# Optimization experiments

Hardware: AMD Instinct MI355X
Metric: run time of the kernel (lower is better)

The kernel has to match this reference:

```python
import jax, jax.numpy as jnp
import numpy as np

B = 1024        # number of dialogs
MX_LEN = 110    # max utterances per dialog (alpha width hardcoded to 110 in source)
G_DIM = 512     # node feature dim
WP, WF = 10, 10 # past / future window
ALPHA_W = 110
NEG = -1e9


def setup_inputs() -> dict:
    key = jax.random.key(0)
    k1, k2, k3 = jax.random.split(key, 3)
    node_features = jax.random.normal(k1, (B, MX_LEN, G_DIM), dtype=jnp.float32)
    var = 2.0 / (G_DIM + G_DIM)  # matches torch init: normal_(0, var)
    weight = jax.random.normal(k2, (G_DIM, G_DIM), dtype=jnp.float32) * var
    text_len = jax.random.randint(k3, (B,), 1, MX_LEN + 1)
    return {"node_features": node_features, "weight": weight, "text_len": text_len}


def reference(node_features, weight, text_len):
    Bsz, L, D = node_features.shape
    # att_matrix[b, l] = weight @ node_features[b, l]
    att = jnp.einsum('de,ble->bld', weight, node_features)            # [B, L, D]
    # score[b, j, l] = att[b, l] . node_features[b, j]
    scores = jnp.einsum('bld,bjd->bjl', att, node_features)           # [B, J, Lkey]
    j = jnp.arange(L)[:, None]   # query position
    l = jnp.arange(L)[None, :]   # key position
    lens = text_len[:, None, None]                                    # [B, 1, 1]
    # window: s = max(0, j-wp), e = min(j+wf, cur_len-1); valid only for j < cur_len
    mask = (l >= j - WP) & (l <= j + WF) & (l <= lens - 1) & (j <= lens - 1)
    probs = jax.nn.softmax(jnp.where(mask, scores, NEG), axis=-1)
    probs = jnp.where(mask, probs, 0.0)                               # [B, L, L]
    # alpha is [mx_len, 110] per batch, zero outside window; stack over batch
    alpha = jnp.zeros((Bsz, L, ALPHA_W), dtype=probs.dtype).at[:, :, :L].set(probs)
    return alpha
```

## Files before the change

### kernel.cpp

```cpp
#include <hip/hip_runtime.h>
#include <stdint.h>

#define L_SZ 110
#define D_SZ 512
#define OUT_W 110
#define A_STRIDE 520
#define C_STRIDE 136
#define A_ROWS 112
#define ATT_ROWS 112
#define G3_ST 40

typedef __attribute__((ext_vector_type(8))) __bf16 bf16x8;
typedef __attribute__((ext_vector_type(4))) __bf16 bf16x4;
typedef __attribute__((ext_vector_type(4))) float f32x4;

__global__ __launch_bounds__(256) void wconv_kernel(const float* __restrict__ W,
                                                    __bf16* __restrict__ wbf) {
    int idx = blockIdx.x * 256 + threadIdx.x;
    float4 w = ((const float4*)W)[idx];
    bf16x4 o;
    o[0] = (__bf16)w.x; o[1] = (__bf16)w.y; o[2] = (__bf16)w.z; o[3] = (__bf16)w.w;
    ((bf16x4*)wbf)[idx] = o;
}

__global__ __launch_bounds__(256, 3) void att_gemm3_kernel(
    const float* __restrict__ nf, const __bf16* __restrict__ wbf,
    const int* __restrict__ tlenp, __bf16* __restrict__ attws)
{
    __shared__ __bf16 A_lds[112 * G3_ST];
    __shared__ __bf16 B_lds[128 * G3_ST];

    const int b   = blockIdx.y;
    const int cg  = blockIdx.x;
    const int tid = threadIdx.x;
    const int lane = tid & 63;
    const int wave = tid >> 6;
    const int l15  = lane & 15;
    const int quad = lane >> 4;

    int len = tlenp[b];
    if (len > L_SZ) len = L_SZ;
    if (len < 1) len = 1;
    const int T = (len + 15) >> 4;
    const int rows_needed = T << 4;

    const float* nfb = nf + (size_t)b * (L_SZ * D_SZ);

    const int r0 = tid >> 2;
    const int c8 = (tid & 3) << 3;
    const int rows2[2] = { r0, r0 + 64 };
    int stat[2];
    #pragma unroll
    for (int s = 0; s < 2; ++s) {
        int r = rows2[s];
        stat[s] = (r >= rows_needed) ? 0 : ((r < L_SZ) ? 1 : 2);
    }

    f32x4 acc[7][2];
    const f32x4 fz = {0.f, 0.f, 0.f, 0.f};
    #pragma unroll
    for (int m = 0; m < 7; ++m) { acc[m][0] = fz; acc[m][1] = fz; }

    float4 abuf[2][2];
    bf16x8 bbuf[2];

    auto load_tiles = [&](int k0) {
        #pragma unroll
        for (int s = 0; s < 2; ++s) {
            if (stat[s] == 1) {
                const float* ap = nfb + (size_t)rows2[s] * D_SZ + k0 + c8;
                abuf[s][0] = *(const float4*)ap;
                abuf[s][1] = *(const float4*)(ap + 4);
            }
            bbuf[s] = *(const bf16x8*)&wbf[(size_t)(cg * 128 + rows2[s]) * D_SZ + k0 + c8];
        }
    };
    auto store_tiles = [&]() {
        #pragma unroll
        for (int s = 0; s < 2; ++s) {
            if (stat[s]) {
                bf16x8 o;
                if (stat[s] == 1) {
                    o[0]=(__bf16)abuf[s][0].x; o[1]=(__bf16)abuf[s][0].y;
                    o[2]=(__bf16)abuf[s][0].z; o[3]=(__bf16)abuf[s][0].w;
                    o[4]=(__bf16)abuf[s][1].x; o[5]=(__bf16)abuf[s][1].y;
                    o[6]=(__bf16)abuf[s][1].z; o[7]=(__bf16)abuf[s][1].w;
                } else {
                    o[0]=o[1]=o[2]=o[3]=o[4]=o[5]=o[6]=o[7]=(__bf16)0.0f;
                }
                *(bf16x8*)&A_lds[rows2[s] * G3_ST + c8] = o;
            }
            *(bf16x8*)&B_lds[rows2[s] * G3_ST + c8] = bbuf[s];
        }
    };

    load_tiles(0);
    for (int kt = 0; kt < 16; ++kt) {
        store_tiles();
        __syncthreads();
        if (kt < 15) load_tiles((kt + 1) << 5);
        bf16x8 bfr[2];
        #pragma unroll
        for (int ni = 0; ni < 2; ++ni)
            bfr[ni] = *(const bf16x8*)&B_lds[(wave * 32 + ni * 16 + l15) * G3_ST + quad * 8];
        #pragma unroll
        for (int m = 0; m < 7; ++m) {
            if (m < T) {
                bf16x8 af = *(const bf16x8*)&A_lds[(m * 16 + l15) * G3_ST + quad * 8];
                acc[m][0] = __builtin_amdgcn_mfma_f32_16x16x32_bf16(af, bfr[0], acc[m][0], 0, 0, 0);
                acc[m][1] = __builtin_amdgcn_mfma_f32_16x16x32_bf16(af, bfr[1], acc[m][1], 0, 0, 0);
            }
        }
        __syncthreads();
    }

    __bf16* tw = &A_lds[wave * 16 * G3_ST];
    const size_t obase = (size_t)b * (ATT_ROWS * D_SZ) + cg * 128 + wave * 32;
    const int erow = lane >> 2;
    const int ec8  = (lane & 3) << 3;
    #pragma unroll
    for (int m = 0; m < 7; ++m) {
        if (m < T) {
            #pragma unroll
            for (int ni = 0; ni < 2; ++ni)
                #pragma unroll
                for (int r = 0; r < 4; ++r)
                    tw[(quad * 4 + r) * G3_ST + ni * 16 + l15] = (__bf16)acc[m][ni][r];
            bf16x8 v = *(const bf16x8*)&tw[erow * G3_ST + ec8];
            *(bf16x8*)&attws[obase + (size_t)(m * 16 + erow) * D_SZ + ec8] = v;
        }
    }
}

__global__ __launch_bounds__(256) void band_kernel(
    const float* __restrict__ nf, const __bf16* __restrict__ attws,
    const int* __restrict__ tlenp, float* __restrict__ out)
{
    const int b = blockIdx.x;
    const int tid = threadIdx.x;
    const int lane = tid & 63;
    const int wave = tid >> 6;
    const int l15 = lane & 15;
    const int quad = lane >> 4;

    int len = tlenp[b];
    if (len > L_SZ) len = L_SZ;
    if (len < 1) len = 1;
    const int T = (len + 15) >> 4;

    const float* nfb = nf + (size_t)b * (L_SZ * D_SZ);
    float* outb = out + (size_t)b * (L_SZ * OUT_W);

    const f32x4 fz = {0.f, 0.f, 0.f, 0.f};
    f32x4 accS[2][3];
    #pragma unroll
    for (int i = 0; i < 2; ++i)
        #pragma unroll
        for (int t = 0; t < 3; ++t) accS[i][t] = fz;

    #pragma unroll
    for (int i = 0; i < 2; ++i) {
        const int tj = wave + (i << 2);
        if (tj < T) {
            int jr = (tj << 4) + l15;
            if (jr > L_SZ - 1) jr = L_SZ - 1;
            const float* ap0 = &nfb[(size_t)jr * D_SZ];
            for (int k0 = 0; k0 < D_SZ; k0 += 32) {
                float4 a0 = *(const float4*)(ap0 + k0 + (quad << 3));
                float4 a1 = *(const float4*)(ap0 + k0 + (quad << 3) + 4);
                bf16x8 af;
                af[0] = (__bf16)a0.x; af[1] = (__bf16)a0.y;
                af[2] = (__bf16)a0.z; af[3] = (__bf16)a0.w;
                af[4] = (__bf16)a1.x; af[5] = (__bf16)a1.y;
                af[6] = (__bf16)a1.z; af[7] = (__bf16)a1.w;
                #pragma unroll
                for (int t = 0; t < 3; ++t) {
                    int tl = tj - 1 + t;
                    if (tl >= 0 && tl < T) {
                        bf16x8 bfr = *(const bf16x8*)&attws[((size_t)b * ATT_ROWS + (tl << 4) + l15) * D_SZ + k0 + (quad << 3)];
                        accS[i][t] = __builtin_amdgcn_mfma_f32_16x16x32_bf16(
                            af, bfr, accS[i][t], 0, 0, 0);
                    }
                }
            }
        }
    }

    #pragma unroll
    for (int i = 0; i < 2; ++i) {
        int tj = wave + 4 * i;
        if (tj >= T) continue;
        #pragma unroll
        for (int r = 0; r < 4; ++r) {
            int j = tj * 16 + quad * 4 + r;
            float v[3]; bool mk[3];
            float vmax = -3.0e38f;
            #pragma unroll
            for (int t = 0; t < 3; ++t) {
                int tl = tj - 1 + t;
                int l = tl * 16 + l15;
                bool in = (tl >= 0) && (tl < T) && (j < len) && (l < len)
                          && (l >= j - 10) && (l <= j + 10);
                float val = in ? accS[i][t][r] : -3.0e38f;
                mk[t] = in; v[t] = val;
                vmax = fmaxf(vmax, val);
            }
            #pragma unroll
            for (int s = 1; s < 16; s <<= 1)
                vmax = fmaxf(vmax, __shfl_xor(vmax, s, 16));
            float e[3]; float esum = 0.f;
            #pragma unroll
            for (int t = 0; t < 3; ++t) {
                e[t] = mk[t] ? __expf(v[t] - vmax) : 0.f;
                esum += e[t];
            }
            #pragma unroll
            for (int s = 1; s < 16; s <<= 1)
                esum += __shfl_xor(esum, s, 16);
            float inv = (esum > 0.f) ? (1.0f / esum) : 0.f;
            if (j < OUT_W) {
                #pragma unroll
                for (int t = 0; t < 3; ++t) {
                    int tl = tj - 1 + t;
                    if (tl >= 0 && tl < T) {
                        int l = tl * 16 + l15;
                        if (l < OUT_W) outb[(size_t)j * OUT_W + l] = e[t] * inv;
                    }
                }
            }
        }
    }
}

__global__ __launch_bounds__(256, 1) void edgeatt_kernel(
    const float* __restrict__ nf, const float* __restrict__ Wf,
    const __bf16* __restrict__ wbf, const int* __restrict__ tlenp,
    float* __restrict__ out, int use_wb)
{
    __shared__ __bf16 A_lds[A_ROWS * A_STRIDE];
    __shared__ __bf16 C_lds[A_ROWS * C_STRIDE];

    const int b = blockIdx.x;
    const int tid = threadIdx.x;
    const int lane = tid & 63;
    const int wave = tid >> 6;
    const int l15 = lane & 15;
    const int quad = lane >> 4;

    int len = tlenp[b];
    if (len > L_SZ) len = L_SZ;
    if (len < 1) len = 1;
    const int T = (len + 15) >> 4;

    const float* nfb = nf + (size_t)b * (L_SZ * D_SZ);
    float* outb = out + (size_t)b * (L_SZ * OUT_W);

    {
        int total4 = len * (D_SZ / 4);
        for (int idx = tid; idx < total4; idx += 256) {
            int row = idx >> 7;
            int c4 = idx & 127;
            float4 v = ((const float4*)nfb)[row * 128 + c4];
            bf16x4 o;
            o[0]=(__bf16)v.x; o[1]=(__bf16)v.y; o[2]=(__bf16)v.z; o[3]=(__bf16)v.w;
            *(bf16x4*)&A_lds[row * A_STRIDE + c4 * 4] = o;
        }
        int zr = 16 * T - len;
        if (zr > 0) {
            int per = A_STRIDE / 4;
            int totalz = zr * per;
            for (int idx = tid; idx < totalz; idx += 256) {
                int row = len + idx / per;
                int c4 = idx % per;
                bf16x4 z; z[0]=z[1]=z[2]=z[3]=(__bf16)0.0f;
                *(bf16x4*)&A_lds[row * A_STRIDE + c4 * 4] = z;
            }
        }
    }
    __syncthreads();

    const int wm = wave >> 1, wn = wave & 1;
    const int h = (T + 1) >> 1;
    const int mt_lo = (wm == 0) ? 0 : h;
    const int nmt = ((wm == 0) ? h : T) - mt_lo;

    const f32x4 fzero = {0.f, 0.f, 0.f, 0.f};
    f32x4 accS[2][3];
    #pragma unroll
    for (int i = 0; i < 2; ++i)
        #pragma unroll
        for (int t = 0; t < 3; ++t) accS[i][t] = fzero;

    for (int c = 0; c < 4; ++c) {
        const int d0 = c * 128;
        f32x4 acc1[4][4];
        #pragma unroll
        for (int mi = 0; mi < 4; ++mi)
            #pragma unroll
            for (int ni = 0; ni < 4; ++ni) acc1[mi][ni] = fzero;

        if (nmt > 0) {
            for (int k0 = 0; k0 < D_SZ; k0 += 32) {
                bf16x8 afrag[4], bfrag[4];
                #pragma unroll
                for (int ni = 0; ni < 4; ++ni) {
                    int d = d0 + (wn * 4 + ni) * 16 + l15;
                    if (use_wb) {
                        bfrag[ni] = *(const bf16x8*)&wbf[(size_t)d * D_SZ + k0 + quad * 8];
                    } else {
                        const float* wp = &Wf[(size_t)d * D_SZ + k0 + quad * 8];
                        float4 w0 = *(const float4*)wp;
                        float4 w1 = *(const float4*)(wp + 4);
                        bf16x8 bb;
                        bb[0]=(__bf16)w0.x; bb[1]=(__bf16)w0.y; bb[2]=(__bf16)w0.z; bb[3]=(__bf16)w0.w;
                        bb[4]=(__bf16)w1.x; bb[5]=(__bf16)w1.y; bb[6]=(__bf16)w1.z; bb[7]=(__bf16)w1.w;
                        bfrag[ni] = bb;
                    }
                }
                #pragma unroll
                for (int mi = 0; mi < 4; ++mi) {
                    if (mi < nmt) {
                        int row = (mt_lo + mi) * 16 + l15;
                        afrag[mi] = *(const bf16x8*)&A_lds[row * A_STRIDE + k0 + quad * 8];
                    }
                }
                #pragma unroll
                for (int mi = 0; mi < 4; ++mi) {
                    if (mi < nmt) {
                        #pragma unroll
                        for (int ni = 0; ni < 4; ++ni)
                            acc1[mi][ni] = __builtin_amdgcn_mfma_f32_16x16x32_bf16(
                                afrag[mi], bfrag[ni], acc1[mi][ni], 0, 0, 0);
                    }
                }
            }
        }
        __syncthreads();

        #pragma unroll
        for (int mi = 0; mi < 4; ++mi) {
            if (mi < nmt) {
                int lbase = (mt_lo + mi) * 16 + quad * 4;
                #pragma unroll
                for (int ni = 0; ni < 4; ++ni) {
                    int dloc = (wn * 4 + ni) * 16 + l15;
                    #pragma unroll
                    for (int r = 0; r < 4; ++r)
                        C_lds[(lbase + r) * C_STRIDE + dloc] = (__bf16)acc1[mi][ni][r];
                }
            }
        }
        __syncthreads();

        for (int kk = 0; kk < 128; kk += 32) {
            #pragma unroll
            for (int i = 0; i < 2; ++i) {
                int tj = wave + 4 * i;
                if (tj < T) {
                    bf16x8 aj = *(const bf16x8*)&A_lds[(tj * 16 + l15) * A_STRIDE + d0 + kk + quad * 8];
                    #pragma unroll
                    for (int t = 0; t < 3; ++t) {
                        int tl = tj - 1 + t;
                        if (tl >= 0 && tl < T) {
                            bf16x8 bj = *(const bf16x8*)&C_lds[(tl * 16 + l15) * C_STRIDE + kk + quad * 8];
                            accS[i][t] = __builtin_amdgcn_mfma_f32_16x16x32_bf16(
                                aj, bj, accS[i][t], 0, 0, 0);
                        }
                    }
                }
            }
        }
        __syncthreads();
    }

    #pragma unroll
    for (int i = 0; i < 2; ++i) {
        int tj = wave + 4 * i;
        if (tj >= T) continue;
        #pragma unroll
        for (int r = 0; r < 4; ++r) {
            int j = tj * 16 + quad * 4 + r;
            float v[3]; bool mk[3];
            float vmax = -3.0e38f;
            #pragma unroll
            for (int t = 0; t < 3; ++t) {
                int tl = tj - 1 + t;
                int l = tl * 16 + l15;
                bool in = (tl >= 0) && (tl < T) && (j < len) && (l < len)
                          && (l >= j - 10) && (l <= j + 10);
                float val = in ? accS[i][t][r] : -3.0e38f;
                mk[t] = in; v[t] = val;
                vmax = fmaxf(vmax, val);
            }
            #pragma unroll
            for (int s = 1; s < 16; s <<= 1)
                vmax = fmaxf(vmax, __shfl_xor(vmax, s, 16));
            float e[3]; float esum = 0.f;
            #pragma unroll
            for (int t = 0; t < 3; ++t) {
                e[t] = mk[t] ? __expf(v[t] - vmax) : 0.f;
                esum += e[t];
            }
            #pragma unroll
            for (int s = 1; s < 16; s <<= 1)
                esum += __shfl_xor(esum, s, 16);
            float inv = (esum > 0.f) ? (1.0f / esum) : 0.f;
            if (j < OUT_W) {
                #pragma unroll
                for (int t = 0; t < 3; ++t) {
                    int tl = tj - 1 + t;
                    if (tl >= 0 && tl < T) {
                        int l = tl * 16 + l15;
                        if (l < OUT_W) outb[(size_t)j * OUT_W + l] = e[t] * inv;
                    }
                }
            }
        }
    }
}

extern "C" void kernel_launch(void* const* d_in, const int* in_sizes, int n_in,
                              void* d_out, int out_size, void* d_ws, size_t ws_size,
                              hipStream_t stream) {
    const float* nf = (const float*)d_in[0];
    const float* W  = (const float*)d_in[1];
    const int* tl   = (const int*)d_in[2];
    float* out      = (float*)d_out;
    __bf16* wbf     = (__bf16*)d_ws;
    const int B = in_sizes[2];

    const size_t wb_bytes  = (size_t)D_SZ * D_SZ * sizeof(__bf16);
    const size_t att_bytes = (size_t)B * ATT_ROWS * D_SZ * sizeof(__bf16);
    const int use_wb = (ws_size >= wb_bytes) ? 1 : 0;
    const int fast   = (use_wb && ws_size >= wb_bytes + att_bytes) ? 1 : 0;

    hipMemsetAsync(d_out, 0, (size_t)out_size * sizeof(float), stream);

    if (use_wb) {
        hipLaunchKernelGGL(wconv_kernel, dim3(256), dim3(256), 0, stream, W, wbf);
    }
    if (fast) {
        __bf16* attws = (__bf16*)((char*)d_ws + wb_bytes);
        hipLaunchKernelGGL(att_gemm3_kernel, dim3(4, B), dim3(256), 0, stream, nf, wbf, tl, attws);
        hipLaunchKernelGGL(band_kernel, dim3(B), dim3(256), 0, stream, nf, attws, tl, out);
    } else {
        hipLaunchKernelGGL(edgeatt_kernel, dim3(B), dim3(256), 0, stream,
                           nf, W, wbf, tl, out, use_wb);
    }
}
```

Before: 449.6 us.

## Pre-convert node features to bf16 and use LDS-free direct-load GEMM kernels

Adds a pass that converts node_features to a zero-padded bf16 workspace copy. New att and band kernels then read MFMA fragments straight from global memory instead of staging fp32 inputs through LDS. The aim is to halve the input bytes the two GEMM stages read and to drop the LDS staging and conversion work inside them. In exchange it adds an extra full read and write of the features plus one more kernel launch, and it needs a larger workspace.

```diff
diff --git a/kernel.cpp b/kernel.cpp
--- a/kernel.cpp
+++ b/kernel.cpp
@@ -8,6 +8,7 @@
 #define C_STRIDE 136
 #define A_ROWS 112
 #define ATT_ROWS 112
+#define NF_ROWS 112
 #define G3_ST 40
 
 typedef __attribute__((ext_vector_type(8))) __bf16 bf16x8;
@@ -21,6 +22,179 @@
     bf16x4 o;
     o[0] = (__bf16)w.x; o[1] = (__bf16)w.y; o[2] = (__bf16)w.z; o[3] = (__bf16)w.w;
     ((bf16x4*)wbf)[idx] = o;
+}
+
+__global__ __launch_bounds__(256) void nfconv_kernel(const float* __restrict__ nf,
+                                                     __bf16* __restrict__ nfbf) {
+    int g = blockIdx.x * 256 + threadIdx.x;
+    int b = g / (NF_ROWS * 64);
+    int rem = g - b * (NF_ROWS * 64);
+    int r = rem >> 6;
+    int c8 = (rem & 63) << 3;
+    bf16x8 o;
+    if (r < L_SZ) {
+        const float* p = nf + ((size_t)b * L_SZ + r) * D_SZ + c8;
+        float4 v0 = *(const float4*)p;
+        float4 v1 = *(const float4*)(p + 4);
+        o[0]=(__bf16)v0.x; o[1]=(__bf16)v0.y; o[2]=(__bf16)v0.z; o[3]=(__bf16)v0.w;
+        o[4]=(__bf16)v1.x; o[5]=(__bf16)v1.y; o[6]=(__bf16)v1.z; o[7]=(__bf16)v1.w;
+    } else {
+        o[0]=o[1]=o[2]=o[3]=o[4]=o[5]=o[6]=o[7]=(__bf16)0.0f;
+    }
+    *(bf16x8*)&nfbf[((size_t)b * NF_ROWS + r) * D_SZ + c8] = o;
+}
+
+__global__ __launch_bounds__(256) void att_direct_kernel(
+    const __bf16* __restrict__ nfbf, const __bf16* __restrict__ wbf,
+    const int* __restrict__ tlenp, __bf16* __restrict__ attws)
+{
+    __shared__ __bf16 tbuf[64 * G3_ST];
+
+    const int b   = blockIdx.y;
+    const int cg  = blockIdx.x;
+    const int tid = threadIdx.x;
+    const int lane = tid & 63;
+    const int wave = tid >> 6;
+    const int l15  = lane & 15;
+    const int quad = lane >> 4;
+
+    int len = tlenp[b];
+    if (len > L_SZ) len = L_SZ;
+    if (len < 1) len = 1;
+    const int T = (len + 15) >> 4;
+
+    const __bf16* arow = nfbf + (size_t)b * (NF_ROWS * D_SZ)
+                              + (size_t)l15 * D_SZ + (quad << 3);
+    const __bf16* brow = wbf + (size_t)(cg * 128 + wave * 32 + l15) * D_SZ + (quad << 3);
+
+    f32x4 acc[7][2];
+    const f32x4 fz = {0.f, 0.f, 0.f, 0.f};
+    #pragma unroll
+    for (int m = 0; m < 7; ++m) { acc[m][0] = fz; acc[m][1] = fz; }
+
+    #pragma unroll 2
+    for (int k0 = 0; k0 < D_SZ; k0 += 32) {
+        bf16x8 bfr0 = *(const bf16x8*)(brow + k0);
+        bf16x8 bfr1 = *(const bf16x8*)(brow + 16 * D_SZ + k0);
+        #pragma unroll
+        for (int m = 0; m < 7; ++m) {
+            if (m < T) {
+                bf16x8 af = *(const bf16x8*)(arow + (size_t)(m * 16) * D_SZ + k0);
+                acc[m][0] = __builtin_amdgcn_mfma_f32_16x16x32_bf16(af, bfr0, acc[m][0], 0, 0, 0);
+                acc[m][1] = __builtin_amdgcn_mfma_f32_16x16x32_bf16(af, bfr1, acc[m][1], 0, 0, 0);
+            }
+        }
+    }
+
+    __bf16* tw = &tbuf[wave * 16 * G3_ST];
+    const size_t obase = (size_t)b * (ATT_ROWS * D_SZ) + cg * 128 + wave * 32;
+    const int erow = lane >> 2;
+    const int ec8  = (lane & 3) << 3;
+    #pragma unroll
+    for (int m = 0; m < 7; ++m) {
+        if (m < T) {
+            #pragma unroll
+            for (int ni = 0; ni < 2; ++ni)
+                #pragma unroll
+                for (int r = 0; r < 4; ++r)
+                    tw[(quad * 4 + r) * G3_ST + ni * 16 + l15] = (__bf16)acc[m][ni][r];
+            bf16x8 v = *(const bf16x8*)&tw[erow * G3_ST + ec8];
+            *(bf16x8*)&attws[obase + (size_t)(m * 16 + erow) * D_SZ + ec8] = v;
+        }
+    }
+}
+
+__global__ __launch_bounds__(256) void band2_kernel(
+    const __bf16* __restrict__ nfbf, const __bf16* __restrict__ attws,
+    const int* __restrict__ tlenp, float* __restrict__ out)
+{
+    const int b = blockIdx.x;
+    const int tid = threadIdx.x;
+    const int lane = tid & 63;
+    const int wave = tid >> 6;
+    const int l15 = lane & 15;
+    const int quad = lane >> 4;
+
+    int len = tlenp[b];
+    if (len > L_SZ) len = L_SZ;
+    if (len < 1) len = 1;
+    const int T = (len + 15) >> 4;
+
+    float* outb = out + (size_t)b * (L_SZ * OUT_W);
+
+    const f32x4 fz = {0.f, 0.f, 0.f, 0.f};
+    f32x4 accS[2][3];
+    #pragma unroll
+    for (int i = 0; i < 2; ++i)
+        #pragma unroll
+        for (int t = 0; t < 3; ++t) accS[i][t] = fz;
+
+    #pragma unroll
+    for (int i = 0; i < 2; ++i) {
+        const int tj = wave + (i << 2);
+        if (tj < T) {
+            int jr = (tj << 4) + l15;
+            if (jr > L_SZ - 1) jr = L_SZ - 1;
+            const __bf16* ap0 = &nfbf[((size_t)b * NF_ROWS + jr) * D_SZ + (quad << 3)];
+            for (int k0 = 0; k0 < D_SZ; k0 += 32) {
+                bf16x8 af = *(const bf16x8*)(ap0 + k0);
+                #pragma unroll
+                for (int t = 0; t < 3; ++t) {
+                    int tl = tj - 1 + t;
+                    if (tl >= 0 && tl < T) {
+                        bf16x8 bfr = *(const bf16x8*)&attws[((size_t)b * ATT_ROWS + (tl << 4) + l15) * D_SZ + k0 + (quad << 3)];
+                        accS[i][t] = __builtin_amdgcn_mfma_f32_16x16x32_bf16(
+                            af, bfr, accS[i][t], 0, 0, 0);
+                    }
+                }
+            }
+        }
+    }
+
+    #pragma unroll
+    for (int i = 0; i < 2; ++i) {
+        int tj = wave + 4 * i;
+        if (tj >= T) continue;
+        #pragma unroll
+        for (int r = 0; r < 4; ++r) {
+            int j = tj * 16 + quad * 4 + r;
+            float v[3]; bool mk[3];
+            float vmax = -3.0e38f;
+            #pragma unroll
+            for (int t = 0; t < 3; ++t) {
+                int tl = tj - 1 + t;
+                int l = tl * 16 + l15;
+                bool in = (tl >= 0) && (tl < T) && (j < len) && (l < len)
+                          && (l >= j - 10) && (l <= j + 10);
+                float val = in ? accS[i][t][r] : -3.0e38f;
+                mk[t] = in; v[t] = val;
+                vmax = fmaxf(vmax, val);
+            }
+            #pragma unroll
+            for (int s = 1; s < 16; s <<= 1)
+                vmax = fmaxf(vmax, __shfl_xor(vmax, s, 16));
+            float e[3]; float esum = 0.f;
+            #pragma unroll
+            for (int t = 0; t < 3; ++t) {
+                e[t] = mk[t] ? __expf(v[t] - vmax) : 0.f;
+                esum += e[t];
+            }
+            #pragma unroll
+            for (int s = 1; s < 16; s <<= 1)
+                esum += __shfl_xor(esum, s, 16);
+            float inv = (esum > 0.f) ? (1.0f / esum) : 0.f;
+            if (j < OUT_W) {
+                #pragma unroll
+                for (int t = 0; t < 3; ++t) {
+                    int tl = tj - 1 + t;
+                    if (tl >= 0 && tl < T) {
+                        int l = tl * 16 + l15;
+                        if (l < OUT_W) outb[(size_t)j * OUT_W + l] = e[t] * inv;
+                    }
+                }
+            }
+        }
+    }
 }
 
 __global__ __launch_bounds__(256, 3) void att_gemm3_kernel(
@@ -431,15 +605,23 @@
 
     const size_t wb_bytes  = (size_t)D_SZ * D_SZ * sizeof(__bf16);
     const size_t att_bytes = (size_t)B * ATT_ROWS * D_SZ * sizeof(__bf16);
+    const size_t nf_bytes  = (size_t)B * NF_ROWS * D_SZ * sizeof(__bf16);
     const int use_wb = (ws_size >= wb_bytes) ? 1 : 0;
     const int fast   = (use_wb && ws_size >= wb_bytes + att_bytes) ? 1 : 0;
+    const int fast2  = (fast && ws_size >= wb_bytes + att_bytes + nf_bytes) ? 1 : 0;
 
     hipMemsetAsync(d_out, 0, (size_t)out_size * sizeof(float), stream);
 
     if (use_wb) {
         hipLaunchKernelGGL(wconv_kernel, dim3(256), dim3(256), 0, stream, W, wbf);
     }
-    if (fast) {
+    if (fast2) {
+        __bf16* attws = (__bf16*)((char*)d_ws + wb_bytes);
+        __bf16* nfbf  = (__bf16*)((char*)d_ws + wb_bytes + att_bytes);
+        hipLaunchKernelGGL(nfconv_kernel, dim3(B * 28), dim3(256), 0, stream, nf, nfbf);
+        hipLaunchKernelGGL(att_direct_kernel, dim3(4, B), dim3(256), 0, stream, nfbf, wbf, tl, attws);
+        hipLaunchKernelGGL(band2_kernel, dim3(B), dim3(256), 0, stream, nfbf, attws, tl, out);
+    } else if (fast) {
         __bf16* attws = (__bf16*)((char*)d_ws + wb_bytes);
         hipLaunchKernelGGL(att_gemm3_kernel, dim3(4, B), dim3(256), 0, stream, nf, wbf, tl, attws);
         hipLaunchKernelGGL(band_kernel, dim3(B), dim3(256), 0, stream, nf, attws, tl, out);
```

Measured after the change: 601.8 us. +33.9%, slower.
